# Kernel optimization log

Measured on AMD Instinct MI355X. Metric: run time of the kernel, lower is better.

Reference implementation:

```python
import jax, jax.numpy as jnp
import numpy as np

H, D = 8, 128           # num_heads, head_dim
HID = 1024              # hidden_size
K = 4                   # short conv kernel
EPS_QK = 1e-6
EPS_NORM = 1e-5


def short_conv(x, w):
    # x: (B, T, C), w: (C, 1, K) depthwise causal conv (zero initial state) + SiLU
    k = w.shape[-1]
    xp = jnp.pad(x, ((0, 0), (k - 1, 0), (0, 0)))
    xc = jnp.transpose(xp, (0, 2, 1))  # (B, C, T+K-1)
    y = jax.lax.conv_general_dilated(xc, w, window_strides=(1,), padding='VALID',
                                     feature_group_count=w.shape[0])
    return jax.nn.silu(jnp.transpose(y, (0, 2, 1)))


def _rmsn(t, eps):
    return t * jax.lax.rsqrt(jnp.mean(t * t, axis=-1, keepdims=True) + eps)


def setup_inputs() -> dict:
    key = jax.random.key(0)
    ks = jax.random.split(key, 16)
    s = 0.02
    inp = {
        'x': jax.random.normal(ks[0], (2, 1024, HID), dtype=jnp.float32),
        'Wq': jax.random.normal(ks[1], (H * D, HID), dtype=jnp.float32) * s,
        'Wk': jax.random.normal(ks[2], (H * D, HID), dtype=jnp.float32) * s,
        'Wv': jax.random.normal(ks[3], (H * D, HID), dtype=jnp.float32) * s,
        'wq_conv': jax.random.normal(ks[4], (H * D, 1, K), dtype=jnp.float32) * 0.3,
        'wk_conv': jax.random.normal(ks[5], (H * D, 1, K), dtype=jnp.float32) * 0.3,
        'wv_conv': jax.random.normal(ks[6], (H * D, 1, K), dtype=jnp.float32) * 0.3,
        'Wfa': jax.random.normal(ks[7], (D, HID), dtype=jnp.float32) * s,
        'Wfb': jax.random.normal(ks[8], (H * D, D), dtype=jnp.float32) * s,
        'Wb': jax.random.normal(ks[9], (H, HID), dtype=jnp.float32) * s,
        'Wga': jax.random.normal(ks[10], (D, HID), dtype=jnp.float32) * s,
        'Wgb': jax.random.normal(ks[11], (H * D, D), dtype=jnp.float32) * s,
        'A_log': jnp.log(jax.random.uniform(ks[12], (H,), minval=1.0, maxval=16.0, dtype=jnp.float32)),
        'dt_bias': jnp.zeros((H, D), dtype=jnp.float32),
        'o_norm_w': jnp.ones((D,), dtype=jnp.float32),
        'Wo': jax.random.normal(ks[13], (HID, H * D), dtype=jnp.float32) * s,
    }
    return inp


def reference(x, Wq, Wk, Wv, wq_conv, wk_conv, wv_conv, Wfa, Wfb, Wb, Wga, Wgb,
              A_log, dt_bias, o_norm_w, Wo):
    B, T, _ = x.shape
    scale = float(D) ** -0.5

    q = short_conv(x @ Wq.T, wq_conv).reshape(B, T, H, D)
    k = short_conv(x @ Wk.T, wk_conv).reshape(B, T, H, D)
    v = short_conv(x @ Wv.T, wv_conv).reshape(B, T, H, D)

    q = (scale ** 2) * _rmsn(q, EPS_QK)
    k = scale * _rmsn(k, EPS_QK)

    a_logits = ((x @ Wfa.T) @ Wfb.T).reshape(B, T, H, D)
    g = -jnp.exp(A_log)[None, None, :, None] * jax.nn.softplus(a_logits + dt_bias)  # (B,T,H,D)
    beta = jax.nn.sigmoid(x @ Wb.T)  # (B,T,H)

    # gated delta-rule recurrence over time; state S: (B, H, Dk, Dv)
    def step(S, inputs):
        q_t, k_t, v_t, g_t, b_t = inputs
        S = S * jnp.exp(g_t)[..., None]                       # per-channel decay on key dim
        kv = jnp.einsum('bhd,bhdv->bhv', k_t, S)              # read
        delta = b_t[..., None] * (v_t - kv)                   # beta-gated delta
        S = S + k_t[..., None] * delta[:, :, None, :]         # rank-1 write
        o = jnp.einsum('bhd,bhdv->bhv', q_t, S)
        return S, o

    tb = lambda t: jnp.moveaxis(t, 1, 0)  # (B,T,...) -> (T,B,...)
    S0 = jnp.zeros((B, H, D, D), dtype=x.dtype)
    _, o_t = jax.lax.scan(step, S0, (tb(q), tb(k), tb(v), tb(g), tb(beta)))
    out = jnp.moveaxis(o_t, 0, 1)  # (B, T, H, D)

    gate = ((x @ Wga.T) @ Wgb.T).reshape(B, T, H, D)
    out = _rmsn(out, EPS_NORM) * o_norm_w * jax.nn.sigmoid(gate)
    return out.reshape(B, T, H * D) @ Wo.T
```

## Files before the change

### kernel.cpp

```cpp
#include <hip/hip_runtime.h>
#include <hip/hip_bf16.h>
#include <math.h>

#define H 8
#define D 128
#define HID 1024
#define KCONV 4

typedef __bf16 bhalf;
typedef __bf16 bhalf4 __attribute__((ext_vector_type(4)));
typedef __bf16 bhalf8 __attribute__((ext_vector_type(8)));
typedef float f32x4 __attribute__((ext_vector_type(4)));
typedef _Float16 hlf;
typedef _Float16 half8 __attribute__((ext_vector_type(8)));
typedef _Float16 half4v __attribute__((ext_vector_type(4)));

__device__ __forceinline__ void async16(const void* g, void* l) {
    __builtin_amdgcn_global_load_lds(
        (const __attribute__((address_space(1))) void*)g,
        (__attribute__((address_space(3))) void*)l, 16, 0, 0);
}

__global__ __launch_bounds__(256) void gemm_bf16_nt(const bhalf* A, const bhalf* B,
                                                    void* Cv,
                                                    int M, int N, int K,
                                                    int lda, int ldb, int ldc, int epi,
                                                    const float* __restrict__ A_log,
                                                    const float* __restrict__ dt_bias,
                                                    const bhalf* A2, const bhalf* B2,
                                                    void* C2, int epi2,
                                                    bhalf* __restrict__ pXAG,
                                                    float* __restrict__ pBETA)
{
    if (blockIdx.z) { A = A2; B = B2; Cv = C2; epi = epi2; }
    __shared__ __align__(16) bhalf As[128][32];
    __shared__ __align__(16) bhalf Bs[64][32];
    int tid = threadIdx.x;
    int wid = tid >> 6, lane = tid & 63;
    int rowBase = blockIdx.y * 128;
    int colBase = blockIdx.x * 64;
    int wm = wid >> 1, wn = wid & 1;

    f32x4 acc[4][2] = {};

    int r = lane >> 2;
    int cseg = lane & 3;

    for (int k0 = 0; k0 < K; k0 += 32) {
        __syncthreads();
#pragma unroll
        for (int s = 0; s < 3; ++s) {
            int j = wid * 3 + s;
            if (j < 8) {
                const bhalf* ga = A + (size_t)(rowBase + j * 16 + r) * lda + k0 + cseg * 8;
                async16(ga, &As[j * 16][0]);
            } else {
                int jb = j - 8;
                const bhalf* ga = B + (size_t)(colBase + jb * 16 + r) * ldb + k0 + cseg * 8;
                async16(ga, &Bs[jb * 16][0]);
            }
        }
        __syncthreads();
        int mq = lane & 15, kq = (lane >> 4) * 8;
        bhalf8 af[4], bfr[2];
#pragma unroll
        for (int mt = 0; mt < 4; ++mt)
            af[mt] = *(const bhalf8*)&As[wm * 64 + mt * 16 + mq][kq];
#pragma unroll
        for (int nt = 0; nt < 2; ++nt)
            bfr[nt] = *(const bhalf8*)&Bs[wn * 32 + nt * 16 + mq][kq];
#pragma unroll
        for (int mt = 0; mt < 4; ++mt)
#pragma unroll
            for (int nt = 0; nt < 2; ++nt)
                acc[mt][nt] = __builtin_amdgcn_mfma_f32_16x16x32_bf16(
                    af[mt], bfr[nt], acc[mt][nt], 0, 0, 0);
    }
    int rquad = (lane >> 4) * 4;
#pragma unroll
    for (int mt = 0; mt < 4; ++mt) {
        int m0 = rowBase + wm * 64 + mt * 16 + rquad;
#pragma unroll
        for (int nt = 0; nt < 2; ++nt) {
            int c = colBase + wn * 32 + (lane & 15) + nt * 16;
#pragma unroll
            for (int rr = 0; rr < 4; ++rr) {
                float val = acc[mt][nt][rr];
                int m = m0 + rr;
                if (epi == 0) {
                    ((float*)Cv)[(size_t)m * ldc + c] = val;
                } else if (epi == 1) {
                    int h = c >> 7, d = c & 127;
                    float z = val + dt_bias[h * D + d];
                    float sp = (z > 20.f) ? z : log1pf(expf(z));
                    ((float*)Cv)[(size_t)m * ldc + c] = expf(-expf(A_log[h]) * sp);
                } else if (epi == 2) {
                    ((bhalf*)Cv)[(size_t)m * ldc + c] = (bhalf)val;
                } else {
                    if (c < 3072) {
                        ((float*)Cv)[(size_t)m * 3072 + c] = val;
                    } else if (c < 3328) {
                        pXAG[(size_t)m * 256 + (c - 3072)] = (bhalf)val;
                    } else if (c < 3336) {
                        pBETA[(size_t)m * 8 + (c - 3328)] = 1.f / (1.f + expf(-val));
                    }
                }
            }
        }
    }
}

__global__ void cast1(const float* __restrict__ s, bhalf* __restrict__ d, int n4)
{
    int i = blockIdx.x * blockDim.x + threadIdx.x;
    if (i >= n4) return;
    float4 v = ((const float4*)s)[i];
    bhalf4 o = {(bhalf)v.x, (bhalf)v.y, (bhalf)v.z, (bhalf)v.w};
    ((bhalf4*)d)[i] = o;
}
__global__ void cast4(const float* __restrict__ s0, const float* __restrict__ s1,
                      const float* __restrict__ s2, const float* __restrict__ s3,
                      bhalf* __restrict__ d0, bhalf* __restrict__ d1,
                      bhalf* __restrict__ d2, bhalf* __restrict__ d3, int n4)
{
    int i = blockIdx.x * blockDim.x + threadIdx.x;
    if (i >= n4) return;
    int a = blockIdx.y;
    const float* s = (a == 0) ? s0 : (a == 1) ? s1 : (a == 2) ? s2 : s3;
    bhalf* d = (a == 0) ? d0 : (a == 1) ? d1 : (a == 2) ? d2 : d3;
    float4 v = ((const float4*)s)[i];
    bhalf4 o = {(bhalf)v.x, (bhalf)v.y, (bhalf)v.z, (bhalf)v.w};
    ((bhalf4*)d)[i] = o;
}

__global__ __launch_bounds__(128) void conv3_kernel(const float* __restrict__ QKV,
                                                    const float* __restrict__ wq,
                                                    const float* __restrict__ wk,
                                                    const float* __restrict__ wv,
                                                    float* __restrict__ Qc,
                                                    float* __restrict__ Kc,
                                                    float* __restrict__ Vc,
                                                    int T)
{
    int which = blockIdx.y;
    const float* w; float* out; int mode; float scale;
    if (which == 0)      { w = wq; out = Qc; mode = 1; scale = 1.0f / 128.0f; }
    else if (which == 1) { w = wk; out = Kc; mode = 1; scale = 0.08838834764831845f; }
    else                 { w = wv; out = Vc; mode = 0; scale = 1.f; }

    int bid = blockIdx.x;
    int h = bid % H;
    int t = (bid / H) % T;
    int b = bid / (H * T);
    int d = threadIdx.x;
    int c = h * D + d;
    const float* base = QKV + (size_t)b * T * 3072 + which * 1024 + c;
    float acc = 0.f;
#pragma unroll
    for (int j = 0; j < KCONV; ++j) {
        int tt = t - (KCONV - 1) + j;
        float xv = (tt >= 0) ? base[(size_t)tt * 3072] : 0.f;
        acc += xv * w[c * KCONV + j];
    }
    float y = acc / (1.f + expf(-acc));
    if (mode) {
        __shared__ float red[2];
        float ss = y * y;
#pragma unroll
        for (int s = 32; s > 0; s >>= 1) ss += __shfl_xor(ss, s, 64);
        if ((threadIdx.x & 63) == 0) red[threadIdx.x >> 6] = ss;
        __syncthreads();
        float tot = red[0] + red[1];
        float r = rsqrtf(tot * (1.f / D) + 1e-6f);
        y = y * r * scale;
    }
    out[(size_t)bid * D + d] = y;
}

template <int CTRL>
__device__ __forceinline__ float dpp_add(float x) {
    int y = __builtin_amdgcn_update_dpp(0, __builtin_bit_cast(int, x),
                                        CTRL, 0xF, 0xF, false);
    return x + __builtin_bit_cast(float, y);
}
__device__ __forceinline__ float wave_sum63(float x) {
    x = dpp_add<0x111>(x);
    x = dpp_add<0x112>(x);
    x = dpp_add<0x114>(x);
    x = dpp_add<0x118>(x);
    x = dpp_add<0x142>(x);
    x = dpp_add<0x143>(x);
    return x;
}


__global__ __launch_bounds__(256) void chunk_prep_kernel(
    const float* __restrict__ Q, const float* __restrict__ K,
    const float* __restrict__ V, const float* __restrict__ E,
    const float* __restrict__ BETA,
    hlf* __restrict__ Wn, float* __restrict__ Uf, hlf* __restrict__ Qt,
    hlf* __restrict__ AoL, hlf* __restrict__ KbT, float* __restrict__ Aend,
    int T)
{
    __shared__ __align__(16) float e_s[32][128];
    __shared__ __align__(16) float k_s[32][128];
    __shared__ __align__(16) float q_s[32][128];
    __shared__ __align__(16) float v_s[32][128];
    __shared__ __align__(16) float U_s[32][128];
    __shared__ __align__(16) hlf  A_s[32][128];
    __shared__ __align__(16) hlf  W_s[32][128];
    __shared__ float P_s[32][32];
    __shared__ float Ao_s[32][32];
    __shared__ float beta_s[32];

    int tid = threadIdx.x, wid = tid >> 6, lane = tid & 63;
    int bid = blockIdx.x;
    int bh = bid >> 5, ch = bid & 31;
    int b = bh >> 3, h = bh & 7;
    int t0 = ch * 32;
    size_t rowb = (size_t)(b * T + t0) * 1024 + h * 128;
    size_t co = (size_t)bh * 32 + ch;

    int rs2 = lane >> 5, seg = (lane & 31) * 4;
#pragma unroll
    for (int p = wid * 4; p < wid * 4 + 4; ++p) {
        int row = p * 2 + rs2;
        async16(E + rowb + (size_t)row * 1024 + seg, &e_s[p * 2][0]);
        async16(K + rowb + (size_t)row * 1024 + seg, &k_s[p * 2][0]);
        async16(Q + rowb + (size_t)row * 1024 + seg, &q_s[p * 2][0]);
        async16(V + rowb + (size_t)row * 1024 + seg, &v_s[p * 2][0]);
    }
    if (wid == 2 && lane < 32)
        beta_s[lane] = BETA[(size_t)(b * T + t0 + lane) * 8 + h];
    __syncthreads();

    for (int x = tid; x < 1024; x += 256) Ao_s[x >> 5][x & 31] = 0.f;
    int d0 = lane * 2;
    if (wid == 0) {
        float a0 = 1.f, a1 = 1.f;
        for (int t = 0; t < 32; ++t) {
            a0 *= e_s[t][d0]; a1 *= e_s[t][d0 + 1];
            A_s[t][d0] = (hlf)a0; A_s[t][d0 + 1] = (hlf)a1;
        }
        Aend[co * 128 + d0] = a0; Aend[co * 128 + d0 + 1] = a1;
    } else if (wid == 1) {
        float s0 = 1.f, s1 = 1.f;
        for (int t = 31; t >= 0; --t) {
            KbT[co * 4096 + (size_t)d0 * 32 + t]       = (hlf)(k_s[t][d0] * s0);
            KbT[co * 4096 + (size_t)(d0 + 1) * 32 + t] = (hlf)(k_s[t][d0 + 1] * s1);
            s0 *= e_s[t][d0]; s1 *= e_s[t][d0 + 1];
        }
    }
    __syncthreads();

#pragma unroll
    for (int ii = 0; ii < 8; ++ii) {
        int i = wid + ii * 4;
        float ki0 = k_s[i][d0], ki1 = k_s[i][d0 + 1];
        float2 qv = *(const float2*)&q_s[i][d0];
        float aa = wave_sum63(qv.x * ki0 + qv.y * ki1);
        if (lane == 63) Ao_s[i][i] = aa;
        float R0 = 1.f, R1 = 1.f;
        for (int j = i - 1; j >= 0; --j) {
            R0 *= e_s[j + 1][d0]; R1 *= e_s[j + 1][d0 + 1];
            float u0 = R0 * k_s[j][d0], u1 = R1 * k_s[j][d0 + 1];
            float pp = wave_sum63(ki0 * u0 + ki1 * u1);
            float a2 = wave_sum63(qv.x * u0 + qv.y * u1);
            if (lane == 63) { P_s[i][j] = pp; Ao_s[i][j] = a2; }
        }
    }
    __syncthreads();

    for (int x = tid; x < 1024; x += 256) {
        int i2 = x >> 5, j2 = x & 31;
        P_s[i2][j2] = (j2 < i2) ? P_s[i2][j2] * beta_s[i2] : 0.f;
    }
    __syncthreads();

    if (wid == 0) {
        for (int i = 0; i < 32; ++i) {
            float bb = beta_s[i];
            float a0 = bb * k_s[i][d0] * (float)A_s[i][d0];
            float a1 = bb * k_s[i][d0 + 1] * (float)A_s[i][d0 + 1];
            for (int k2 = 0; k2 < i; ++k2) {
                float L = P_s[i][k2];
                a0 -= L * (float)W_s[k2][d0];
                a1 -= L * (float)W_s[k2][d0 + 1];
            }
            W_s[i][d0] = (hlf)a0; W_s[i][d0 + 1] = (hlf)a1;
        }
    } else if (wid == 1) {
        for (int i = 0; i < 32; ++i) {
            float bb = beta_s[i];
            float2 vv = *(const float2*)&v_s[i][d0];
            float a0 = bb * vv.x, a1 = bb * vv.y;
            for (int k2 = 0; k2 < i; ++k2) {
                float L = P_s[i][k2];
                a0 -= L * U_s[k2][d0];
                a1 -= L * U_s[k2][d0 + 1];
            }
            U_s[i][d0] = a0; U_s[i][d0 + 1] = a1;
        }
    } else {
        for (int r2 = wid - 2; r2 < 32; r2 += 2) {
            float2 qv = *(const float2*)&q_s[r2][d0];
            Qt[co * 4096 + (size_t)r2 * 128 + d0]     = (hlf)(qv.x * (float)A_s[r2][d0]);
            Qt[co * 4096 + (size_t)r2 * 128 + d0 + 1] = (hlf)(qv.y * (float)A_s[r2][d0 + 1]);
        }
    }
    __syncthreads();

    for (int x = tid; x < 4096; x += 256) {
        Wn[co * 4096 + x] = (hlf)(-(float)W_s[x >> 7][x & 127]);
        Uf[co * 4096 + x] = U_s[x >> 7][x & 127];
    }
    for (int x = tid; x < 1024; x += 256)
        AoL[co * 1024 + x] = (hlf)Ao_s[x >> 5][x & 31];
}

struct ScanOps {
    half8 aw0, aw1, aw2, aw3;
    half8 aq0, aq1, aq2, aq3;
    half8 bK0, bK1, bK2, bK3;
    half8 aA;
    float u0, u1, u2, u3;
    float ae0, ae1, ae2, ae3;
};

__device__ __forceinline__ void scan_load(ScanOps& o, size_t co,
    const hlf* __restrict__ Wn, const float* __restrict__ Uf,
    const hlf* __restrict__ Qt, const hlf* __restrict__ Ao,
    const hlf* __restrict__ KbT, const float* __restrict__ Aend,
    int tr, int vc, int dh2, int mq, int kq, int rq, int v0)
{
    const hlf*   Wc  = Wn  + co * 4096;
    const hlf*   Qc  = Qt  + co * 4096;
    const hlf*   Aoc = Ao  + co * 1024;
    const hlf*   Kbc = KbT + co * 4096;
    const float* Uc  = Uf  + co * 4096;
    const float* Aec = Aend + co * 128;
    size_t rw = (size_t)(tr + mq) * 128 + kq;
    o.aw0 = *(const half8*)&Wc[rw];
    o.aw1 = *(const half8*)&Wc[rw + 32];
    o.aw2 = *(const half8*)&Wc[rw + 64];
    o.aw3 = *(const half8*)&Wc[rw + 96];
    o.aq0 = *(const half8*)&Qc[rw];
    o.aq1 = *(const half8*)&Qc[rw + 32];
    o.aq2 = *(const half8*)&Qc[rw + 64];
    o.aq3 = *(const half8*)&Qc[rw + 96];
    o.aA  = *(const half8*)&Aoc[(tr + mq) * 32 + kq];
    o.bK0 = *(const half8*)&Kbc[(size_t)(dh2 + mq) * 32 + kq];
    o.bK1 = *(const half8*)&Kbc[(size_t)(dh2 + 16 + mq) * 32 + kq];
    o.bK2 = *(const half8*)&Kbc[(size_t)(dh2 + 32 + mq) * 32 + kq];
    o.bK3 = *(const half8*)&Kbc[(size_t)(dh2 + 48 + mq) * 32 + kq];
    size_t ru = (size_t)(tr + rq) * 128 + v0 + vc + mq;
    o.u0 = Uc[ru];
    o.u1 = Uc[ru + 128];
    o.u2 = Uc[ru + 256];
    o.u3 = Uc[ru + 384];
    o.ae0 = Aec[dh2 + mq];
    o.ae1 = Aec[dh2 + 16 + mq];
    o.ae2 = Aec[dh2 + 32 + mq];
    o.ae3 = Aec[dh2 + 48 + mq];
}

__device__ __forceinline__ void scan_body(const ScanOps& o, int c,
    float (*SfR)[132], hlf (*ShR)[136], float (*SfW)[132], hlf (*ShW)[136],
    hlf (*Dt)[40], float* __restrict__ O,
    int b, int h, int v0, int T,
    int tr, int vc, int vr2, int dh2, int mq, int kq, int rq)
{
    half8 bs0 = *(const half8*)&ShR[vc + mq][kq];
    half8 bs1 = *(const half8*)&ShR[vc + mq][32 + kq];
    half8 bs2 = *(const half8*)&ShR[vc + mq][64 + kq];
    half8 bs3 = *(const half8*)&ShR[vc + mq][96 + kq];

    f32x4 dacc = {o.u0, o.u1, o.u2, o.u3};
    dacc = __builtin_amdgcn_mfma_f32_16x16x32_f16(o.aw0, bs0, dacc, 0, 0, 0);
    dacc = __builtin_amdgcn_mfma_f32_16x16x32_f16(o.aw1, bs1, dacc, 0, 0, 0);
    dacc = __builtin_amdgcn_mfma_f32_16x16x32_f16(o.aw2, bs2, dacc, 0, 0, 0);
    dacc = __builtin_amdgcn_mfma_f32_16x16x32_f16(o.aw3, bs3, dacc, 0, 0, 0);
    half4v dh4 = {(hlf)dacc[0], (hlf)dacc[1], (hlf)dacc[2], (hlf)dacc[3]};
    *(half4v*)&Dt[vc + mq][tr + rq] = dh4;

    asm volatile("s_waitcnt lgkmcnt(0)" ::: "memory");
    __builtin_amdgcn_s_barrier();
    __builtin_amdgcn_sched_barrier(0);

    f32x4 oacc = {0.f, 0.f, 0.f, 0.f};
    oacc = __builtin_amdgcn_mfma_f32_16x16x32_f16(o.aq0, bs0, oacc, 0, 0, 0);
    oacc = __builtin_amdgcn_mfma_f32_16x16x32_f16(o.aq1, bs1, oacc, 0, 0, 0);
    oacc = __builtin_amdgcn_mfma_f32_16x16x32_f16(o.aq2, bs2, oacc, 0, 0, 0);
    oacc = __builtin_amdgcn_mfma_f32_16x16x32_f16(o.aq3, bs3, oacc, 0, 0, 0);
    half8 bD = *(const half8*)&Dt[vc + mq][kq];
    oacc = __builtin_amdgcn_mfma_f32_16x16x32_f16(o.aA, bD, oacc, 0, 0, 0);
    size_t ob = ((size_t)(b * T + c * 32 + tr + rq) * 8 + h) * 128 + v0 + vc + mq;
    O[ob]        = oacc[0];
    O[ob + 1024] = oacc[1];
    O[ob + 2048] = oacc[2];
    O[ob + 3072] = oacc[3];

    half8 aD = *(const half8*)&Dt[vr2 + mq][kq];
    int dc0 = dh2 + mq, dc1 = dh2 + 16 + mq, dc2 = dh2 + 32 + mq, dc3 = dh2 + 48 + mq;
    f32x4 s0, s1, s2, s3;
#pragma unroll
    for (int rr = 0; rr < 4; ++rr) {
        s0[rr] = SfR[vr2 + rq + rr][dc0] * o.ae0;
        s1[rr] = SfR[vr2 + rq + rr][dc1] * o.ae1;
        s2[rr] = SfR[vr2 + rq + rr][dc2] * o.ae2;
        s3[rr] = SfR[vr2 + rq + rr][dc3] * o.ae3;
    }
    s0 = __builtin_amdgcn_mfma_f32_16x16x32_f16(aD, o.bK0, s0, 0, 0, 0);
    s1 = __builtin_amdgcn_mfma_f32_16x16x32_f16(aD, o.bK1, s1, 0, 0, 0);
    s2 = __builtin_amdgcn_mfma_f32_16x16x32_f16(aD, o.bK2, s2, 0, 0, 0);
    s3 = __builtin_amdgcn_mfma_f32_16x16x32_f16(aD, o.bK3, s3, 0, 0, 0);
#pragma unroll
    for (int rr = 0; rr < 4; ++rr) {
        SfW[vr2 + rq + rr][dc0] = s0[rr];  ShW[vr2 + rq + rr][dc0] = (hlf)s0[rr];
        SfW[vr2 + rq + rr][dc1] = s1[rr];  ShW[vr2 + rq + rr][dc1] = (hlf)s1[rr];
        SfW[vr2 + rq + rr][dc2] = s2[rr];  ShW[vr2 + rq + rr][dc2] = (hlf)s2[rr];
        SfW[vr2 + rq + rr][dc3] = s3[rr];  ShW[vr2 + rq + rr][dc3] = (hlf)s3[rr];
    }
    asm volatile("s_waitcnt lgkmcnt(0)" ::: "memory");
    __builtin_amdgcn_s_barrier();
    __builtin_amdgcn_sched_barrier(0);
}

__global__ __launch_bounds__(256, 1) void chunk_scan_kernel(
    const hlf* __restrict__ Wn, const float* __restrict__ Uf,
    const hlf* __restrict__ Qt, const hlf* __restrict__ Ao,
    const hlf* __restrict__ KbT, const float* __restrict__ Aend,
    float* __restrict__ O, int T)
{
    __shared__ __align__(16) float Sf0[32][132], Sf1[32][132];
    __shared__ __align__(16) hlf  Sh0[32][136], Sh1[32][136];
    __shared__ __align__(16) hlf  Dt[32][40];

    int tid = threadIdx.x, wid = tid >> 6, lane = tid & 63;
    int nbh = gridDim.x >> 2;
    int bh = blockIdx.x % nbh, vs = blockIdx.x / nbh;
    int b = bh >> 3, h = bh & 7;
    int v0 = vs * 32;

    for (int r = wid; r < 32; r += 4) {
        for (int c2 = lane; c2 < 132; c2 += 64) Sf0[r][c2] = 0.f;
        for (int c2 = lane; c2 < 136; c2 += 64) Sh0[r][c2] = (hlf)0.f;
    }

    int mq = lane & 15, kq = (lane >> 4) * 8, rq = (lane >> 4) * 4;
    int tr = (wid >> 1) * 16, vc = (wid & 1) * 16;
    int vr2 = (wid >> 1) * 16, dh2 = (wid & 1) * 64;

    int NC = T / 32;
    size_t cb = (size_t)bh * 32;
    ScanOps opA, opB;
    scan_load(opA, cb, Wn, Uf, Qt, Ao, KbT, Aend, tr, vc, dh2, mq, kq, rq, v0);
    __syncthreads();

    for (int cc = 0; cc < NC; cc += 2) {
        scan_load(opB, cb + cc + 1, Wn, Uf, Qt, Ao, KbT, Aend,
                  tr, vc, dh2, mq, kq, rq, v0);
        scan_body(opA, cc, Sf0, Sh0, Sf1, Sh1, Dt, O, b, h, v0, T,
                  tr, vc, vr2, dh2, mq, kq, rq);
        if (cc + 2 < NC)
            scan_load(opA, cb + cc + 2, Wn, Uf, Qt, Ao, KbT, Aend,
                      tr, vc, dh2, mq, kq, rq, v0);
        scan_body(opB, cc + 1, Sf1, Sh1, Sf0, Sh0, Dt, O, b, h, v0, T,
                  tr, vc, vr2, dh2, mq, kq, rq);
    }
}

__global__ __launch_bounds__(128) void outnorm_kernel(const float* __restrict__ O,
                                                      const float* __restrict__ GATE,
                                                      const float* __restrict__ w,
                                                      bhalf* __restrict__ Obf)
{
    int bid = blockIdx.x;
    int d = threadIdx.x;
    size_t base = (size_t)bid * D;
    float y = O[base + d];
    __shared__ float red[2];
    float ss = y * y;
#pragma unroll
    for (int s = 32; s > 0; s >>= 1) ss += __shfl_xor(ss, s, 64);
    if ((threadIdx.x & 63) == 0) red[threadIdx.x >> 6] = ss;
    __syncthreads();
    float tot = red[0] + red[1];
    float r = rsqrtf(tot * (1.f / D) + 1e-5f);
    float gz = GATE[base + d];
    float sg = 1.f / (1.f + expf(-gz));
    Obf[base + d] = (bhalf)(y * r * w[d] * sg);
}

extern "C" void kernel_launch(void* const* d_in, const int* in_sizes, int n_in,
                              void* d_out, int out_size, void* d_ws, size_t ws_size,
                              hipStream_t stream)
{
    const float* x       = (const float*)d_in[0];
    const float* Wq      = (const float*)d_in[1];
    const float* Wk      = (const float*)d_in[2];
    const float* Wv      = (const float*)d_in[3];
    const float* wq_conv = (const float*)d_in[4];
    const float* wk_conv = (const float*)d_in[5];
    const float* wv_conv = (const float*)d_in[6];
    const float* Wfa     = (const float*)d_in[7];
    const float* Wfb     = (const float*)d_in[8];
    const float* Wb      = (const float*)d_in[9];
    const float* Wga     = (const float*)d_in[10];
    const float* Wgb     = (const float*)d_in[11];
    const float* A_log   = (const float*)d_in[12];
    const float* dt_bias = (const float*)d_in[13];
    const float* o_norm_w= (const float*)d_in[14];
    const float* Wo      = (const float*)d_in[15];

    int BT = in_sizes[0] / HID;
    int T = 1024;
    int B_ = BT / T;
    size_t M = (size_t)BT;
    size_t sz_big = M * HID;
    const int nW = HID * HID;
    const int nS = D * HID;
    const int NCAT = 3392;

    float* fp = (float*)d_ws;
    float* QKVp = fp;               fp += 3 * sz_big;
    float* Qc   = fp;               fp += sz_big;
    float* Kc   = fp;               fp += sz_big;
    float* Vc   = fp;               fp += sz_big;
    float* EGb  = fp;               fp += sz_big;
    float* GATE = fp;               fp += sz_big;
    float* Obuf = fp;               fp += sz_big;
    float* BETA = fp;               fp += M * H;
    bhalf* bp = (bhalf*)fp;
    bhalf* xb   = bp;               bp += sz_big;
    bhalf* Wcat = bp;               bp += (size_t)NCAT * HID;
    bhalf* Wob  = bp;               bp += nW;
    bhalf* Wfbb = bp;               bp += nS;
    bhalf* Wgbb = bp;               bp += nS;
    bhalf* XAG  = bp;               bp += M * 256;
    bhalf* Obf  = bp;               bp += sz_big;

    dim3 blk(256);

    cast1<<<(int)((sz_big / 4 + 255) / 256), 256, 0, stream>>>(x, xb, (int)(sz_big / 4));
    cast4<<<dim3((nW / 4 + 255) / 256, 4), 256, 0, stream>>>(Wq, Wk, Wv, Wo,
        Wcat, Wcat + nW, Wcat + 2 * (size_t)nW, Wob, nW / 4);
    cast4<<<dim3((nS / 4 + 255) / 256, 4), 256, 0, stream>>>(Wfa, Wga, Wfb, Wgb,
        Wcat + 3 * (size_t)nW, Wcat + 3 * (size_t)nW + nS, Wfbb, Wgbb, nS / 4);
    cast1<<<(H * HID / 4 + 255) / 256, 256, 0, stream>>>(Wb,
        Wcat + 3 * (size_t)nW + 2 * (size_t)nS, H * HID / 4);

    gemm_bf16_nt<<<dim3(NCAT / 64, BT / 128), blk, 0, stream>>>(
        xb, Wcat, QKVp, BT, NCAT, HID, HID, HID, 3072, 3, nullptr, nullptr,
        nullptr, nullptr, nullptr, 0, XAG, BETA);

    conv3_kernel<<<dim3(BT * H, 3), 128, 0, stream>>>(QKVp,
                                                      wq_conv, wk_conv, wv_conv,
                                                      Qc, Kc, Vc, T);

    gemm_bf16_nt<<<dim3(HID / 64, BT / 128, 2), blk, 0, stream>>>(
        XAG, Wfbb, EGb, BT, HID, D, 256, D, HID, 1, A_log, dt_bias,
        XAG + D, Wgbb, GATE, 0, nullptr, nullptr);

    int nbh = B_ * 8;
    float* Uf   = QKVp;
    float* Aend = Uf + (size_t)nbh * 32 * 4096;
    hlf* Wn  = (hlf*)(Aend + (size_t)nbh * 32 * 128);
    hlf* Qt  = Wn  + (size_t)nbh * 32 * 4096;
    hlf* AoLp= Qt  + (size_t)nbh * 32 * 4096;
    hlf* KbT = AoLp + (size_t)nbh * 32 * 1024;

    chunk_prep_kernel<<<nbh * 32, 256, 0, stream>>>(Qc, Kc, Vc, EGb, BETA,
                                                    Wn, Uf, Qt, AoLp, KbT, Aend, T);
    chunk_scan_kernel<<<nbh * 4, 256, 0, stream>>>(Wn, Uf, Qt, AoLp, KbT, Aend,
                                                   Obuf, T);

    outnorm_kernel<<<BT * H, 128, 0, stream>>>(Obuf, GATE, o_norm_w, Obf);

    gemm_bf16_nt<<<dim3(HID / 64, BT / 128), blk, 0, stream>>>(
        Obf, Wob, (float*)d_out, BT, HID, HID, HID, HID, HID, 0, nullptr, nullptr,
        nullptr, nullptr, nullptr, 0, nullptr, nullptr);
}
```

Before: 352.3 us.

## Keep scan state in registers, split output by v-slice, trim prep LDS

The chunk scan kernel now keeps the fp32 recurrent state in per-wave MFMA accumulator registers instead of double-buffered fp32/fp16 LDS tiles, computing the transposed update so each wave owns a fixed state tile. Only an fp16 copy is written to LDS for the read MFMAs. The output buffer is relaid out per 32-wide v-slice, and outnorm gathers from that layout. The prep kernel drops its Q/V LDS staging and reads those values directly from global memory. This cuts LDS traffic and footprint, in exchange for extra registers and uncoalesced global reads in the prep kernel.

After: 319.8 us. 9.2% less time.

```diff
diff --git a/kernel.cpp b/kernel.cpp
--- a/kernel.cpp
+++ b/kernel.cpp
@@ -204,8 +204,6 @@
 {
     __shared__ __align__(16) float e_s[32][128];
     __shared__ __align__(16) float k_s[32][128];
-    __shared__ __align__(16) float q_s[32][128];
-    __shared__ __align__(16) float v_s[32][128];
     __shared__ __align__(16) float U_s[32][128];
     __shared__ __align__(16) hlf  A_s[32][128];
     __shared__ __align__(16) hlf  W_s[32][128];
@@ -227,14 +225,12 @@
         int row = p * 2 + rs2;
         async16(E + rowb + (size_t)row * 1024 + seg, &e_s[p * 2][0]);
         async16(K + rowb + (size_t)row * 1024 + seg, &k_s[p * 2][0]);
-        async16(Q + rowb + (size_t)row * 1024 + seg, &q_s[p * 2][0]);
-        async16(V + rowb + (size_t)row * 1024 + seg, &v_s[p * 2][0]);
-    }
+    }
+    __syncthreads();
+
+    for (int x = tid; x < 1024; x += 256) Ao_s[x >> 5][x & 31] = 0.f;
     if (wid == 2 && lane < 32)
         beta_s[lane] = BETA[(size_t)(b * T + t0 + lane) * 8 + h];
-    __syncthreads();
-
-    for (int x = tid; x < 1024; x += 256) Ao_s[x >> 5][x & 31] = 0.f;
     int d0 = lane * 2;
     if (wid == 0) {
         float a0 = 1.f, a1 = 1.f;
@@ -257,7 +253,7 @@
     for (int ii = 0; ii < 8; ++ii) {
         int i = wid + ii * 4;
         float ki0 = k_s[i][d0], ki1 = k_s[i][d0 + 1];
-        float2 qv = *(const float2*)&q_s[i][d0];
+        float2 qv = *(const float2*)(Q + rowb + (size_t)i * 1024 + d0);
         float aa = wave_sum63(qv.x * ki0 + qv.y * ki1);
         if (lane == 63) Ao_s[i][i] = aa;
         float R0 = 1.f, R1 = 1.f;
@@ -292,7 +288,7 @@
     } else if (wid == 1) {
         for (int i = 0; i < 32; ++i) {
             float bb = beta_s[i];
-            float2 vv = *(const float2*)&v_s[i][d0];
+            float2 vv = *(const float2*)(V + rowb + (size_t)i * 1024 + d0);
             float a0 = bb * vv.x, a1 = bb * vv.y;
             for (int k2 = 0; k2 < i; ++k2) {
                 float L = P_s[i][k2];
@@ -303,7 +299,7 @@
         }
     } else {
         for (int r2 = wid - 2; r2 < 32; r2 += 2) {
-            float2 qv = *(const float2*)&q_s[r2][d0];
+            float2 qv = *(const float2*)(Q + rowb + (size_t)r2 * 1024 + d0);
             Qt[co * 4096 + (size_t)r2 * 128 + d0]     = (hlf)(qv.x * (float)A_s[r2][d0]);
             Qt[co * 4096 + (size_t)r2 * 128 + d0 + 1] = (hlf)(qv.y * (float)A_s[r2][d0 + 1]);
         }
@@ -324,14 +320,14 @@
     half8 bK0, bK1, bK2, bK3;
     half8 aA;
     float u0, u1, u2, u3;
-    float ae0, ae1, ae2, ae3;
+    f32x4 ae0, ae1, ae2, ae3;
 };
 
 __device__ __forceinline__ void scan_load(ScanOps& o, size_t co,
     const hlf* __restrict__ Wn, const float* __restrict__ Uf,
     const hlf* __restrict__ Qt, const hlf* __restrict__ Ao,
     const hlf* __restrict__ KbT, const float* __restrict__ Aend,
-    int tr, int vc, int dh2, int mq, int kq, int rq, int v0)
+    int tr, int vc, int dseg, int mq, int kq, int rq, int v0)
 {
     const hlf*   Wc  = Wn  + co * 4096;
     const hlf*   Qc  = Qt  + co * 4096;
@@ -349,31 +345,30 @@
     o.aq2 = *(const half8*)&Qc[rw + 64];
     o.aq3 = *(const half8*)&Qc[rw + 96];
     o.aA  = *(const half8*)&Aoc[(tr + mq) * 32 + kq];
-    o.bK0 = *(const half8*)&Kbc[(size_t)(dh2 + mq) * 32 + kq];
-    o.bK1 = *(const half8*)&Kbc[(size_t)(dh2 + 16 + mq) * 32 + kq];
-    o.bK2 = *(const half8*)&Kbc[(size_t)(dh2 + 32 + mq) * 32 + kq];
-    o.bK3 = *(const half8*)&Kbc[(size_t)(dh2 + 48 + mq) * 32 + kq];
+    o.bK0 = *(const half8*)&Kbc[(size_t)(dseg + mq) * 32 + kq];
+    o.bK1 = *(const half8*)&Kbc[(size_t)(dseg + 16 + mq) * 32 + kq];
+    o.bK2 = *(const half8*)&Kbc[(size_t)(dseg + 32 + mq) * 32 + kq];
+    o.bK3 = *(const half8*)&Kbc[(size_t)(dseg + 48 + mq) * 32 + kq];
     size_t ru = (size_t)(tr + rq) * 128 + v0 + vc + mq;
     o.u0 = Uc[ru];
     o.u1 = Uc[ru + 128];
     o.u2 = Uc[ru + 256];
     o.u3 = Uc[ru + 384];
-    o.ae0 = Aec[dh2 + mq];
-    o.ae1 = Aec[dh2 + 16 + mq];
-    o.ae2 = Aec[dh2 + 32 + mq];
-    o.ae3 = Aec[dh2 + 48 + mq];
+    o.ae0 = *(const f32x4*)&Aec[dseg + rq];
+    o.ae1 = *(const f32x4*)&Aec[dseg + 16 + rq];
+    o.ae2 = *(const f32x4*)&Aec[dseg + 32 + rq];
+    o.ae3 = *(const f32x4*)&Aec[dseg + 48 + rq];
 }
 
 __device__ __forceinline__ void scan_body(const ScanOps& o, int c,
-    float (*SfR)[132], hlf (*ShR)[136], float (*SfW)[132], hlf (*ShW)[136],
-    hlf (*Dt)[40], float* __restrict__ O,
-    int b, int h, int v0, int T,
-    int tr, int vc, int vr2, int dh2, int mq, int kq, int rq)
-{
-    half8 bs0 = *(const half8*)&ShR[vc + mq][kq];
-    half8 bs1 = *(const half8*)&ShR[vc + mq][32 + kq];
-    half8 bs2 = *(const half8*)&ShR[vc + mq][64 + kq];
-    half8 bs3 = *(const half8*)&ShR[vc + mq][96 + kq];
+    f32x4* sreg, hlf (*Sh)[136], hlf (*Dt)[40], float* __restrict__ O,
+    int b, int h, int v0s, int T, int Mrows,
+    int tr, int vc, int vtile, int dseg, int mq, int kq, int rq)
+{
+    half8 bs0 = *(const half8*)&Sh[vc + mq][kq];
+    half8 bs1 = *(const half8*)&Sh[vc + mq][32 + kq];
+    half8 bs2 = *(const half8*)&Sh[vc + mq][64 + kq];
+    half8 bs3 = *(const half8*)&Sh[vc + mq][96 + kq];
 
     f32x4 dacc = {o.u0, o.u1, o.u2, o.u3};
     dacc = __builtin_amdgcn_mfma_f32_16x16x32_f16(o.aw0, bs0, dacc, 0, 0, 0);
@@ -394,32 +389,32 @@
     oacc = __builtin_amdgcn_mfma_f32_16x16x32_f16(o.aq3, bs3, oacc, 0, 0, 0);
     half8 bD = *(const half8*)&Dt[vc + mq][kq];
     oacc = __builtin_amdgcn_mfma_f32_16x16x32_f16(o.aA, bD, oacc, 0, 0, 0);
-    size_t ob = ((size_t)(b * T + c * 32 + tr + rq) * 8 + h) * 128 + v0 + vc + mq;
-    O[ob]        = oacc[0];
-    O[ob + 1024] = oacc[1];
-    O[ob + 2048] = oacc[2];
-    O[ob + 3072] = oacc[3];
-
-    half8 aD = *(const half8*)&Dt[vr2 + mq][kq];
-    int dc0 = dh2 + mq, dc1 = dh2 + 16 + mq, dc2 = dh2 + 32 + mq, dc3 = dh2 + 48 + mq;
-    f32x4 s0, s1, s2, s3;
-#pragma unroll
-    for (int rr = 0; rr < 4; ++rr) {
-        s0[rr] = SfR[vr2 + rq + rr][dc0] * o.ae0;
-        s1[rr] = SfR[vr2 + rq + rr][dc1] * o.ae1;
-        s2[rr] = SfR[vr2 + rq + rr][dc2] * o.ae2;
-        s3[rr] = SfR[vr2 + rq + rr][dc3] * o.ae3;
-    }
-    s0 = __builtin_amdgcn_mfma_f32_16x16x32_f16(aD, o.bK0, s0, 0, 0, 0);
-    s1 = __builtin_amdgcn_mfma_f32_16x16x32_f16(aD, o.bK1, s1, 0, 0, 0);
-    s2 = __builtin_amdgcn_mfma_f32_16x16x32_f16(aD, o.bK2, s2, 0, 0, 0);
-    s3 = __builtin_amdgcn_mfma_f32_16x16x32_f16(aD, o.bK3, s3, 0, 0, 0);
-#pragma unroll
-    for (int rr = 0; rr < 4; ++rr) {
-        SfW[vr2 + rq + rr][dc0] = s0[rr];  ShW[vr2 + rq + rr][dc0] = (hlf)s0[rr];
-        SfW[vr2 + rq + rr][dc1] = s1[rr];  ShW[vr2 + rq + rr][dc1] = (hlf)s1[rr];
-        SfW[vr2 + rq + rr][dc2] = s2[rr];  ShW[vr2 + rq + rr][dc2] = (hlf)s2[rr];
-        SfW[vr2 + rq + rr][dc3] = s3[rr];  ShW[vr2 + rq + rr][dc3] = (hlf)s3[rr];
+    size_t ob = (size_t)v0s * Mrows * 256 +
+                ((size_t)(b * T + c * 32 + tr + rq) * 8 + h) * 32 + vc + mq;
+    O[ob]       = oacc[0];
+    O[ob + 256] = oacc[1];
+    O[ob + 512] = oacc[2];
+    O[ob + 768] = oacc[3];
+
+    half8 aD = *(const half8*)&Dt[vtile + mq][kq];
+    f32x4 s0 = sreg[0] * o.ae0;
+    f32x4 s1 = sreg[1] * o.ae1;
+    f32x4 s2 = sreg[2] * o.ae2;
+    f32x4 s3 = sreg[3] * o.ae3;
+    s0 = __builtin_amdgcn_mfma_f32_16x16x32_f16(o.bK0, aD, s0, 0, 0, 0);
+    s1 = __builtin_amdgcn_mfma_f32_16x16x32_f16(o.bK1, aD, s1, 0, 0, 0);
+    s2 = __builtin_amdgcn_mfma_f32_16x16x32_f16(o.bK2, aD, s2, 0, 0, 0);
+    s3 = __builtin_amdgcn_mfma_f32_16x16x32_f16(o.bK3, aD, s3, 0, 0, 0);
+    sreg[0] = s0; sreg[1] = s1; sreg[2] = s2; sreg[3] = s3;
+    {
+        half4v h0 = {(hlf)s0[0], (hlf)s0[1], (hlf)s0[2], (hlf)s0[3]};
+        half4v h1 = {(hlf)s1[0], (hlf)s1[1], (hlf)s1[2], (hlf)s1[3]};
+        half4v h2 = {(hlf)s2[0], (hlf)s2[1], (hlf)s2[2], (hlf)s2[3]};
+        half4v h3 = {(hlf)s3[0], (hlf)s3[1], (hlf)s3[2], (hlf)s3[3]};
+        *(half4v*)&Sh[vtile + mq][dseg + rq]      = h0;
+        *(half4v*)&Sh[vtile + mq][dseg + 16 + rq] = h1;
+        *(half4v*)&Sh[vtile + mq][dseg + 32 + rq] = h2;
+        *(half4v*)&Sh[vtile + mq][dseg + 48 + rq] = h3;
     }
     asm volatile("s_waitcnt lgkmcnt(0)" ::: "memory");
     __builtin_amdgcn_s_barrier();
@@ -432,8 +427,7 @@
     const hlf* __restrict__ KbT, const float* __restrict__ Aend,
     float* __restrict__ O, int T)
 {
-    __shared__ __align__(16) float Sf0[32][132], Sf1[32][132];
-    __shared__ __align__(16) hlf  Sh0[32][136], Sh1[32][136];
+    __shared__ __align__(16) hlf  Sh[32][136];
     __shared__ __align__(16) hlf  Dt[32][40];
 
     int tid = threadIdx.x, wid = tid >> 6, lane = tid & 63;
@@ -441,44 +435,45 @@
     int bh = blockIdx.x % nbh, vs = blockIdx.x / nbh;
     int b = bh >> 3, h = bh & 7;
     int v0 = vs * 32;
-
-    for (int r = wid; r < 32; r += 4) {
-        for (int c2 = lane; c2 < 132; c2 += 64) Sf0[r][c2] = 0.f;
-        for (int c2 = lane; c2 < 136; c2 += 64) Sh0[r][c2] = (hlf)0.f;
-    }
+    int Mrows = (nbh >> 3) * T;
+
+    for (int x = tid; x < 32 * 136; x += 256) ((hlf*)Sh)[x] = (hlf)0.f;
 
     int mq = lane & 15, kq = (lane >> 4) * 8, rq = (lane >> 4) * 4;
     int tr = (wid >> 1) * 16, vc = (wid & 1) * 16;
-    int vr2 = (wid >> 1) * 16, dh2 = (wid & 1) * 64;
+    int vtile = (wid >> 1) * 16, dseg = (wid & 1) * 64;
+
+    f32x4 sreg[4] = {};
 
     int NC = T / 32;
     size_t cb = (size_t)bh * 32;
     ScanOps opA, opB;
-    scan_load(opA, cb, Wn, Uf, Qt, Ao, KbT, Aend, tr, vc, dh2, mq, kq, rq, v0);
+    scan_load(opA, cb, Wn, Uf, Qt, Ao, KbT, Aend, tr, vc, dseg, mq, kq, rq, v0);
     __syncthreads();
 
     for (int cc = 0; cc < NC; cc += 2) {
         scan_load(opB, cb + cc + 1, Wn, Uf, Qt, Ao, KbT, Aend,
-                  tr, vc, dh2, mq, kq, rq, v0);
-        scan_body(opA, cc, Sf0, Sh0, Sf1, Sh1, Dt, O, b, h, v0, T,
-                  tr, vc, vr2, dh2, mq, kq, rq);
+                  tr, vc, dseg, mq, kq, rq, v0);
+        scan_body(opA, cc, sreg, Sh, Dt, O, b, h, vs, T, Mrows,
+                  tr, vc, vtile, dseg, mq, kq, rq);
         if (cc + 2 < NC)
             scan_load(opA, cb + cc + 2, Wn, Uf, Qt, Ao, KbT, Aend,
-                      tr, vc, dh2, mq, kq, rq, v0);
-        scan_body(opB, cc + 1, Sf1, Sh1, Sf0, Sh0, Dt, O, b, h, v0, T,
-                  tr, vc, vr2, dh2, mq, kq, rq);
+                      tr, vc, dseg, mq, kq, rq, v0);
+        scan_body(opB, cc + 1, sreg, Sh, Dt, O, b, h, vs, T, Mrows,
+                  tr, vc, vtile, dseg, mq, kq, rq);
     }
 }
 
 __global__ __launch_bounds__(128) void outnorm_kernel(const float* __restrict__ O,
                                                       const float* __restrict__ GATE,
                                                       const float* __restrict__ w,
-                                                      bhalf* __restrict__ Obf)
+                                                      bhalf* __restrict__ Obf,
+                                                      int Mrows)
 {
     int bid = blockIdx.x;
     int d = threadIdx.x;
     size_t base = (size_t)bid * D;
-    float y = O[base + d];
+    float y = O[(size_t)(d >> 5) * Mrows * 256 + (size_t)bid * 32 + (d & 31)];
     __shared__ float red[2];
     float ss = y * y;
 #pragma unroll
@@ -575,7 +570,7 @@
     chunk_scan_kernel<<<nbh * 4, 256, 0, stream>>>(Wn, Uf, Qt, AoLp, KbT, Aend,
                                                    Obuf, T);
 
-    outnorm_kernel<<<BT * H, 128, 0, stream>>>(Obuf, GATE, o_norm_w, Obf);
+    outnorm_kernel<<<BT * H, 128, 0, stream>>>(Obuf, GATE, o_norm_w, Obf, BT);
 
     gemm_bf16_nt<<<dim3(HID / 64, BT / 128), blk, 0, stream>>>(
         Obf, Wob, (float*)d_out, BT, HID, HID, HID, HID, HID, 0, nullptr, nullptr,
```
